# Performance work log

Hardware: AMD Instinct MI355X
Metric: run time of the kernel (lower is better)

The kernel has to match this reference:

```python
import jax, jax.numpy as jnp
import numpy as np

WINDOWS = [2, 4, 6]
THR = 0.5


def conv1x1(x, w, b):
    # x: [N,C,H,W], w: [O,C], b: [O]
    return jnp.einsum('nchw,oc->nohw', x, w) + b[None, :, None, None]


def cpool(x):
    # channel max + mean -> [N,2,H,W]
    return jnp.stack([x.max(axis=1), x.mean(axis=1)], axis=1)


def mask_fusion(orin, feature, w1, b1, w2, b2):
    sim = jax.nn.sigmoid(jnp.sum(conv1x1(cpool(orin), w1, b1) * conv1x1(cpool(feature), w2, b2), axis=1, keepdims=True))
    mask = (sim > THR).astype(orin.dtype)
    return mask * feature + (1.0 - mask) * orin


def unfold(x, kh, kw, sh, sw, w):
    # torch F.unfold equivalent -> [N, C*kh*kw, w*w] (channel-major like torch)
    rows = jnp.arange(w)[:, None] * sh + jnp.arange(kh)[None, :]  # [w,kh]
    cols = jnp.arange(w)[:, None] * sw + jnp.arange(kw)[None, :]  # [w,kw]
    p = x[:, :, rows[:, :, None, None], cols[None, None, :, :]]  # [N,C,w,kh,w,kw]
    p = p.transpose(0, 1, 3, 5, 2, 4)  # [N,C,kh,kw,w,w]
    N, C = x.shape[:2]
    return p.reshape(N, C * kh * kw, w * w)


def fold(cols_, H, W, kh, kw, sh, sw, w):
    # torch F.fold equivalent (col2im with overlap-add)
    N, CK, P = cols_.shape
    C = CK // (kh * kw)
    p = cols_.reshape(N, C, kh, kw, w, w).transpose(0, 1, 4, 2, 5, 3).reshape(N, C, w * kh, w * kw)
    r = (jnp.arange(w)[:, None] * sh + jnp.arange(kh)[None, :]).reshape(-1)
    c = (jnp.arange(w)[:, None] * sw + jnp.arange(kw)[None, :]).reshape(-1)
    return jnp.zeros((N, C, H, W), cols_.dtype).at[:, :, r[:, None], c[None, :]].add(p)


def psa(u, wq, wk, wv):
    # u: [N,C,P,L]; scaled dot-product self-attention over L within each patch
    t = u.transpose(0, 2, 3, 1)  # [N,P,L,C]
    q, k, v = t @ wq, t @ wk, t @ wv
    s = jnp.einsum('nplc,npmc->nplm', q, k) / jnp.sqrt(jnp.asarray(t.shape[-1], t.dtype))
    o = jnp.einsum('nplm,npmc->nplc', jax.nn.softmax(s, axis=-1), v)
    return o.transpose(0, 3, 1, 2)


def setup_inputs():
    key = jax.random.key(0)
    ks = jax.random.split(key, 20)
    N, C, H, W = 4, 64, 72, 72
    E = len(WINDOWS) * C
    nrm = lambda k, shape, s: jax.random.normal(k, shape, jnp.float32) * s
    return {
        'x': nrm(ks[0], (N, C, H, W), 1.0),
        'exp_w': nrm(ks[1], (E, C), C ** -0.5), 'exp_b': jnp.zeros((E,), jnp.float32),
        'res_w': nrm(ks[2], (C, E), E ** -0.5), 'res_b': jnp.zeros((C,), jnp.float32),
        'fus_w': nrm(ks[3], (C, C), C ** -0.5), 'fus_b': jnp.zeros((C,), jnp.float32),
        'wq': nrm(ks[4], (C, C), C ** -0.5),
        'wk': nrm(ks[5], (C, C), C ** -0.5),
        'wv': nrm(ks[6], (C, C), C ** -0.5),
        'mf1a_w': nrm(ks[7], (2, 2), 0.7), 'mf1a_b': jnp.zeros((2,), jnp.float32),
        'mf1b_w': nrm(ks[8], (2, 2), 0.7), 'mf1b_b': jnp.zeros((2,), jnp.float32),
        'mf2a_w': nrm(ks[9], (2, 2), 0.7), 'mf2a_b': jnp.zeros((2,), jnp.float32),
        'mf2b_w': nrm(ks[10], (2, 2), 0.7), 'mf2b_b': jnp.zeros((2,), jnp.float32),
    }


def reference(x, exp_w, exp_b, res_w, res_b, fus_w, fus_b, wq, wk, wv,
              mf1a_w, mf1a_b, mf1b_w, mf1b_b, mf2a_w, mf2a_b, mf2b_w, mf2b_b):
    N, C, H, W = x.shape
    expx = conv1x1(x, exp_w, exp_b)  # [N, 3C, H, W]
    parts = jnp.split(expx, len(WINDOWS), axis=1)
    outs = []
    for i, w in enumerate(WINDOWS):
        sh, sw = H // w, W // w
        kh, kw = sh + H % w, sw + W % w
        u = unfold(parts[i], kh, kw, sh, sw, w)       # [N, C*kh*kw, w*w]
        u = u.reshape(N, C, w * w, kh * kw)           # raw reinterpret, as in torch .view
        a = psa(u, wq, wk, wv).reshape(N, C * kh * kw, w * w)
        cnt = fold(jnp.ones_like(a), H, W, kh, kw, sh, sw, w)
        outs.append(fold(a, H, W, kh, kw, sh, sw, w) / cnt)
    out = mask_fusion(jnp.concatenate(outs, axis=1), expx, mf1a_w, mf1a_b, mf1b_w, mf1b_b)
    out = conv1x1(out, res_w, res_b)
    out = mask_fusion(out, x, mf2a_w, mf2a_b, mf2b_w, mf2b_b)
    return conv1x1(out, fus_w, fus_b)
```

## Files before the change

### kernel.cpp

```cpp
#include <hip/hip_runtime.h>

constexpr int CN = 4;
constexpr int CC = 64;
constexpr int CH = 72, CW = 72;
constexpr int HW = CH * CW;
constexpr int NPOS = CN * HW;
constexpr long TOKF = 3L * NPOS * 64;
constexpr long HPAD = 4096;

typedef _Float16 h4 __attribute__((ext_vector_type(4)));
typedef _Float16 h8 __attribute__((ext_vector_type(8)));
typedef float f4 __attribute__((ext_vector_type(4)));

__device__ __forceinline__ int fidx(int row, int g, int off) {
  return (row << 6) + ((g ^ (row & 7)) << 3) + off;
}
__device__ __forceinline__ int f192(int row, int g) {
  return row * 192 + (((g & 24) | ((g ^ row) & 7)) << 3);
}

template <int WW, int SS>
__device__ __forceinline__ void expand_body(const float* __restrict__ x,
                                            const float* __restrict__ w64,
                                            const float* __restrict__ b64,
                                            float* __restrict__ out, int pg) {
  int n = pg / HW;
  int pos = pg - n * HW;
  int h = pos / CW, wcol = pos % CW;

  float xv[64];
  const float* xp = x + (long)n * CC * HW + pos;
#pragma unroll
  for (int c = 0; c < 64; ++c) xv[c] = xp[c * HW];

  int wr = h / SS, kx = h % SS, wcq = wcol / SS, ky = wcol % SS;
  int j = kx * (SS * WW * WW) + ky * (WW * WW) + wr * WW + wcq;
  float* op = out + ((long)n * HW + j) * 64;

#pragma unroll 1
  for (int og = 0; og < 16; ++og) {
    float t0[4];
#pragma unroll
    for (int i = 0; i < 4; ++i) {
      int o = og * 4 + i;
      float acc = b64[o];
      const float* wp = w64 + o * 64;
#pragma unroll
      for (int cg = 0; cg < 16; ++cg) {
        float4 w4 = *(const float4*)(wp + 4 * cg);
        acc = fmaf(xv[4 * cg + 0], w4.x, acc);
        acc = fmaf(xv[4 * cg + 1], w4.y, acc);
        acc = fmaf(xv[4 * cg + 2], w4.z, acc);
        acc = fmaf(xv[4 * cg + 3], w4.w, acc);
      }
      t0[i] = acc;
    }
    *(float4*)(op + og * 4) = make_float4(t0[0], t0[1], t0[2], t0[3]);
  }
}

__global__ __launch_bounds__(256) void k_prep(
    const float* __restrict__ x, const float* __restrict__ exp_w,
    const float* __restrict__ exp_b, const float* __restrict__ wq,
    const float* __restrict__ wk, const float* __restrict__ wv,
    const float* __restrict__ res_w, const float* __restrict__ fus_w,
    float* __restrict__ ex, _Float16* __restrict__ wTh,
    _Float16* __restrict__ wTl, _Float16* __restrict__ rwh,
    _Float16* __restrict__ rwl, _Float16* __restrict__ fwh,
    _Float16* __restrict__ fwl) {
  int b = blockIdx.x;
  if (b >= 243) {
    int i = (b - 243) * 256 + threadIdx.x;
    float v;
    _Float16 *dh, *dl;
    int off;
    if (i < 12288) {
      int m = i >> 12;
      int r = i & 4095;
      int cp = r >> 6, c = r & 63;
      const float* src = (m == 0) ? wq : ((m == 1) ? wk : wv);
      v = src[c * 64 + cp];
      dh = wTh; dl = wTl; off = i;
    } else if (i < 24576) {
      off = i - 12288;
      v = res_w[off];
      dh = rwh; dl = rwl;
    } else {
      off = i - 24576;
      v = fus_w[off];
      dh = fwh; dl = fwl;
    }
    _Float16 h = (_Float16)v;
    dh[off] = h;
    dl[off] = (_Float16)(v - (float)h);
    return;
  }
  int wi = b / 81;
  int pg = (b - wi * 81) * 256 + threadIdx.x;
  if (wi == 0)
    expand_body<2, 36>(x, exp_w, exp_b, ex, pg);
  else if (wi == 1)
    expand_body<4, 18>(x, exp_w + 4096, exp_b + 64, ex + (long)NPOS * 64, pg);
  else
    expand_body<6, 12>(x, exp_w + 8192, exp_b + 128, ex + 2L * NPOS * 64, pg);
}

__global__ __launch_bounds__(256) void k_qkv(
    const float* __restrict__ ex, const _Float16* __restrict__ wTh,
    const _Float16* __restrict__ wTl, _Float16* __restrict__ qh,
    _Float16* __restrict__ ql, _Float16* __restrict__ kh,
    _Float16* __restrict__ kl, _Float16* __restrict__ vth,
    _Float16* __restrict__ vtl) {
  __shared__ __align__(16) _Float16 Wh[12288], Wl[12288];
  __shared__ __align__(16) float Cb[4096];
  _Float16* Eh = (_Float16*)Cb;
  _Float16* El = (_Float16*)Cb + 4096;

  const int tid = threadIdx.x;
  const long tok0 = (long)blockIdx.x * 64;
  const int lane = tid & 63, w = tid >> 6;
  const int lw = lane & 15, lg = lane >> 4;

  {
    int srow = tid >> 2, sfq = tid & 3;
#pragma unroll
    for (int p = 0; p < 4; ++p) {
      int c0 = (4 * p + sfq) * 4;
      float4 v = *(const float4*)(ex + (tok0 + srow) * 64 + c0);
      h4 hh = {(_Float16)v.x, (_Float16)v.y, (_Float16)v.z, (_Float16)v.w};
      h4 ll = {(_Float16)(v.x - (float)hh[0]), (_Float16)(v.y - (float)hh[1]),
               (_Float16)(v.z - (float)hh[2]), (_Float16)(v.w - (float)hh[3])};
      *(h4*)&Eh[fidx(srow, c0 >> 3, c0 & 7)] = hh;
      *(h4*)&El[fidx(srow, c0 >> 3, c0 & 7)] = ll;
    }
  }
#pragma unroll
  for (int it = 0; it < 6; ++it) {
    int idx = it * 256 + tid;
    int row = idx >> 3, gr = idx & 7;
    *(h8*)&Wh[fidx(row, gr, 0)] = *(const h8*)(wTh + idx * 8);
    *(h8*)&Wl[fidx(row, gr, 0)] = *(const h8*)(wTl + idx * 8);
  }
  __syncthreads();

  h8 eh[2], el[2];
#pragma unroll
  for (int s = 0; s < 2; ++s) {
    eh[s] = *(const h8*)&Eh[fidx(w * 16 + lw, s * 4 + lg, 0)];
    el[s] = *(const h8*)&El[fidx(w * 16 + lw, s * 4 + lg, 0)];
  }
  __syncthreads();

  const float SC = 0.125f * 1.4426950408889634f;
#pragma unroll 1
  for (int p = 0; p < 3; ++p) {
#pragma unroll
    for (int ot = 0; ot < 4; ++ot) {
      f4 acc = (f4){0.f, 0.f, 0.f, 0.f};
#pragma unroll
      for (int s = 0; s < 2; ++s) {
        h8 bh = *(const h8*)&Wh[fidx(p * 64 + ot * 16 + lw, s * 4 + lg, 0)];
        h8 bl = *(const h8*)&Wl[fidx(p * 64 + ot * 16 + lw, s * 4 + lg, 0)];
        acc = __builtin_amdgcn_mfma_f32_16x16x32_f16(eh[s], bh, acc, 0, 0, 0);
        acc = __builtin_amdgcn_mfma_f32_16x16x32_f16(el[s], bh, acc, 0, 0, 0);
        acc = __builtin_amdgcn_mfma_f32_16x16x32_f16(eh[s], bl, acc, 0, 0, 0);
      }
#pragma unroll
      for (int r = 0; r < 4; ++r) {
        int row = w * 16 + 4 * lg + r;
        int col = ot * 16 + lw;
        Cb[(row << 6) + ((((col >> 2) ^ (row & 15))) << 2) + (col & 3)] =
            acc[r];
      }
    }
    __syncthreads();

    if (p < 2) {
      int tokl = tid >> 2, off = (tid & 3) * 16;
      float vals[16];
#pragma unroll
      for (int j = 0; j < 4; ++j) {
        int slot = (off >> 2) + j;
        f4 v = *(const f4*)&Cb[(tokl << 6) + (((slot ^ (tokl & 15))) << 2)];
        vals[4 * j + 0] = v[0]; vals[4 * j + 1] = v[1];
        vals[4 * j + 2] = v[2]; vals[4 * j + 3] = v[3];
      }
      float sc = (p == 0) ? SC : 1.0f;
      _Float16* dh = (p == 0 ? qh : kh) + (tok0 + tokl) * 64 + off;
      _Float16* dl = (p == 0 ? ql : kl) + (tok0 + tokl) * 64 + off;
      h8 hh0, hh1, ll0, ll1;
#pragma unroll
      for (int j = 0; j < 8; ++j) {
        float x0 = vals[j] * sc;
        _Float16 h = (_Float16)x0;
        hh0[j] = h;
        ll0[j] = (_Float16)(x0 - (float)h);
        float x1 = vals[8 + j] * sc;
        _Float16 h1 = (_Float16)x1;
        hh1[j] = h1;
        ll1[j] = (_Float16)(x1 - (float)h1);
      }
      *(h8*)dh = hh0; *(h8*)(dh + 8) = hh1;
      *(h8*)dl = ll0; *(h8*)(dl + 8) = ll1;
    } else {
      int ch0 = (tid & 15) * 4, tokl0 = (tid >> 4) * 4;
      float tv[4][4];
#pragma unroll
      for (int r = 0; r < 4; ++r) {
        int row = tokl0 + r;
        int slot = (ch0 >> 2) ^ (row & 15);
        f4 v = *(const f4*)&Cb[(row << 6) + (slot << 2)];
        tv[r][0] = v[0]; tv[r][1] = v[1]; tv[r][2] = v[2]; tv[r][3] = v[3];
      }
      long tokg = tok0 + tokl0;
      int wi = (int)(tokg / NPOS);
      long tl = tokg - (long)wi * NPOS;
      int L = (wi == 0) ? 1296 : ((wi == 1) ? 324 : 144);
      int g = (int)(tl / L);
      int key0 = (int)(tl - (long)g * L);
      long base = (long)wi * NPOS * 64 + (long)g * 64 * L + key0;
#pragma unroll
      for (int i = 0; i < 4; ++i) {
        h4 hh, ll;
#pragma unroll
        for (int r = 0; r < 4; ++r) {
          _Float16 h = (_Float16)tv[r][i];
          hh[r] = h;
          ll[r] = (_Float16)(tv[r][i] - (float)h);
        }
        *(h4*)&vth[base + (long)(ch0 + i) * L] = hh;
        *(h4*)&vtl[base + (long)(ch0 + i) * L] = ll;
      }
    }
    __syncthreads();
  }
}

__global__ __launch_bounds__(256) void k_attn(
    const _Float16* __restrict__ qg, const _Float16* __restrict__ qgl,
    const _Float16* __restrict__ kg, const _Float16* __restrict__ kgl,
    const _Float16* __restrict__ vg, const _Float16* __restrict__ vgl,
    float* __restrict__ og_) {
  __shared__ __align__(16) _Float16 Qh[4096], Ql[4096];
  __shared__ __align__(16) _Float16 Kh[4096], Kl[4096];
  __shared__ __align__(16) _Float16 Vh[4096], Vl[4096];
  __shared__ __align__(16) _Float16 Ph[4096], Pl[4096];

  const int tid = threadIdx.x;
  int b = blockIdx.x;
  int L, g, qt, NCH;
  long tokbase, vbase;
  if (b < 336) {
    L = 1296; NCH = 21; g = b / 21; qt = b - g * 21;
    tokbase = (long)g * 1296;
    vbase = (long)g * 64 * 1296;
  } else if (b < 720) {
    int t = b - 336;
    L = 324; NCH = 6; g = t / 6; qt = t - g * 6;
    tokbase = (long)NPOS + (long)g * 324;
    vbase = (long)NPOS * 64 + (long)g * 64 * 324;
  } else {
    int t = b - 720;
    L = 144; NCH = 3; g = t / 3; qt = t - g * 3;
    tokbase = 2L * NPOS + (long)g * 144;
    vbase = 2L * NPOS * 64 + (long)g * 64 * 144;
  }

  const int lane = tid & 63, w = tid >> 6;
  const int lw = lane & 15, lg = lane >> 4;
  const int w16 = w * 16;

#pragma unroll
  for (int it = 0; it < 2; ++it) {
    int idx = it * 256 + tid;
    int row = idx >> 3, gr = idx & 7;
    long src = (tokbase + qt * 64 + row) * 64 + gr * 8;
    *(h8*)&Qh[fidx(row, gr, 0)] = *(const h8*)(qg + src);
    *(h8*)&Ql[fidx(row, gr, 0)] = *(const h8*)(qgl + src);
  }

  float m_s = -1e30f, l_s = 0.f;
  f4 oa[4];
#pragma unroll
  for (int i = 0; i < 4; ++i) oa[i] = (f4){0.f, 0.f, 0.f, 0.f};

  h8 rk0, rk1, rl0, rl1, rv0, rv1, rw0, rw1;
  auto loadKV = [&](int chn) {
    {
      int idx = tid;
      int row = idx >> 3, gr = idx & 7;
      long ks = (tokbase + chn * 64 + row) * 64 + gr * 8;
      long vs = vbase + (long)row * L + chn * 64 + gr * 8;
      rk0 = *(const h8*)(kg + ks);
      rl0 = *(const h8*)(kgl + ks);
      rv0 = *(const h8*)(vg + vs);
      rw0 = *(const h8*)(vgl + vs);
    }
    {
      int idx = 256 + tid;
      int row = idx >> 3, gr = idx & 7;
      long ks = (tokbase + chn * 64 + row) * 64 + gr * 8;
      long vs = vbase + (long)row * L + chn * 64 + gr * 8;
      rk1 = *(const h8*)(kg + ks);
      rl1 = *(const h8*)(kgl + ks);
      rv1 = *(const h8*)(vg + vs);
      rw1 = *(const h8*)(vgl + vs);
    }
  };
  loadKV(0);

  for (int ch = 0; ch < NCH; ++ch) {
    __syncthreads();
    {
      int row = tid >> 3, gr = tid & 7;
      *(h8*)&Kh[fidx(row, gr, 0)] = rk0;
      *(h8*)&Kl[fidx(row, gr, 0)] = rl0;
      *(h8*)&Vh[fidx(row, gr, 0)] = rv0;
      *(h8*)&Vl[fidx(row, gr, 0)] = rw0;
      int row1 = (256 + tid) >> 3;
      *(h8*)&Kh[fidx(row1, gr, 0)] = rk1;
      *(h8*)&Kl[fidx(row1, gr, 0)] = rl1;
      *(h8*)&Vh[fidx(row1, gr, 0)] = rv1;
      *(h8*)&Vl[fidx(row1, gr, 0)] = rw1;
    }
    __syncthreads();
    if (ch + 1 < NCH) loadKV(ch + 1);

    f4 sa[4];
#pragma unroll
    for (int kt = 0; kt < 4; ++kt) sa[kt] = (f4){0.f, 0.f, 0.f, 0.f};
#pragma unroll
    for (int slab = 0; slab < 2; ++slab) {
      h8 qbh = *(const h8*)&Qh[fidx(w16 + lw, slab * 4 + lg, 0)];
      h8 qbl = *(const h8*)&Ql[fidx(w16 + lw, slab * 4 + lg, 0)];
#pragma unroll
      for (int kt = 0; kt < 4; ++kt) {
        h8 ah = *(const h8*)&Kh[fidx(kt * 16 + lw, slab * 4 + lg, 0)];
        h8 al = *(const h8*)&Kl[fidx(kt * 16 + lw, slab * 4 + lg, 0)];
        sa[kt] = __builtin_amdgcn_mfma_f32_16x16x32_f16(ah, qbh, sa[kt], 0, 0, 0);
        sa[kt] = __builtin_amdgcn_mfma_f32_16x16x32_f16(al, qbh, sa[kt], 0, 0, 0);
        sa[kt] = __builtin_amdgcn_mfma_f32_16x16x32_f16(ah, qbl, sa[kt], 0, 0, 0);
      }
    }

    float pr[4][4];
    float pmax = -1e30f;
#pragma unroll
    for (int kt = 0; kt < 4; ++kt)
#pragma unroll
      for (int r = 0; r < 4; ++r) {
        int kidx = ch * 64 + kt * 16 + 4 * lg + r;
        float s = (kidx < L) ? sa[kt][r] : -1e30f;
        pr[kt][r] = s;
        pmax = fmaxf(pmax, s);
      }
    pmax = fmaxf(pmax, __shfl_xor(pmax, 16));
    pmax = fmaxf(pmax, __shfl_xor(pmax, 32));
    float mn = fmaxf(m_s, pmax);
    float fs = exp2f(m_s - mn);
    m_s = mn;
    float rs = 0.f;
#pragma unroll
    for (int kt = 0; kt < 4; ++kt)
#pragma unroll
      for (int r = 0; r < 4; ++r) {
        float e = exp2f(pr[kt][r] - mn);
        pr[kt][r] = e;
        rs += e;
      }
    rs += __shfl_xor(rs, 16);
    rs += __shfl_xor(rs, 32);
    l_s = l_s * fs + rs;
    float fsb[4];
#pragma unroll
    for (int r = 0; r < 4; ++r) fsb[r] = __shfl(fs, 4 * lg + r);
#pragma unroll
    for (int ct = 0; ct < 4; ++ct)
#pragma unroll
      for (int r = 0; r < 4; ++r) oa[ct][r] *= fsb[r];

#pragma unroll
    for (int kt = 0; kt < 4; ++kt) {
      h4 hh = {(_Float16)pr[kt][0], (_Float16)pr[kt][1], (_Float16)pr[kt][2],
               (_Float16)pr[kt][3]};
      h4 ll = {(_Float16)(pr[kt][0] - (float)hh[0]),
               (_Float16)(pr[kt][1] - (float)hh[1]),
               (_Float16)(pr[kt][2] - (float)hh[2]),
               (_Float16)(pr[kt][3] - (float)hh[3])};
      int key0 = kt * 16 + 4 * lg;
      int kgr = key0 >> 3, ko = key0 & 7;
      *(h4*)&Ph[fidx(w16 + lw, kgr, ko)] = hh;
      *(h4*)&Pl[fidx(w16 + lw, kgr, ko)] = ll;
    }

#pragma unroll
    for (int slab = 0; slab < 2; ++slab) {
      h8 pah = *(const h8*)&Ph[fidx(w16 + lw, slab * 4 + lg, 0)];
      h8 pal = *(const h8*)&Pl[fidx(w16 + lw, slab * 4 + lg, 0)];
#pragma unroll
      for (int ct = 0; ct < 4; ++ct) {
        h8 vbh = *(const h8*)&Vh[fidx(ct * 16 + lw, slab * 4 + lg, 0)];
        h8 vbl = *(const h8*)&Vl[fidx(ct * 16 + lw, slab * 4 + lg, 0)];
        oa[ct] = __builtin_amdgcn_mfma_f32_16x16x32_f16(pah, vbh, oa[ct], 0, 0, 0);
        oa[ct] = __builtin_amdgcn_mfma_f32_16x16x32_f16(pal, vbh, oa[ct], 0, 0, 0);
        oa[ct] = __builtin_amdgcn_mfma_f32_16x16x32_f16(pah, vbl, oa[ct], 0, 0, 0);
      }
    }
  }

  float linv[4];
#pragma unroll
  for (int r = 0; r < 4; ++r) linv[r] = 1.0f / __shfl(l_s, 4 * lg + r);
#pragma unroll
  for (int r = 0; r < 4; ++r) {
    int qi = qt * 64 + w16 + 4 * lg + r;
    if (qi < L) {
      float* op = og_ + (tokbase + qi) * 64 + lw;
#pragma unroll
      for (int ct = 0; ct < 4; ++ct) op[ct * 16] = oa[ct][r] * linv[r];
    }
  }
}

__global__ __launch_bounds__(256) void k_maskA(
    const float* __restrict__ ex, const float* __restrict__ att,
    const float* __restrict__ m1aw, const float* __restrict__ m1ab,
    const float* __restrict__ m1bw, const float* __restrict__ m1bb,
    _Float16* __restrict__ f1h, _Float16* __restrict__ f1l) {
  const int tid = threadIdx.x;
  const int wv = tid >> 6, lane = tid & 63;
  int pg = blockIdx.x * 4 + wv;
  int n = pg / HW, posn = pg - n * HW;
  int h = posn / CW, wcol = posn % CW;
  auto tok = [&](int S, int W) -> int {
    int wr = h / S, kx = h % S, wcq = wcol / S, ky = wcol % S;
    return kx * (S * W * W) + ky * (W * W) + wr * W + wcq;
  };
  int j0 = tok(36, 2), j1 = tok(18, 4), j2 = tok(12, 6);
  long t0 = ((long)n * HW + j0) * 64 + lane;
  long t1 = ((long)NPOS + (long)n * HW + j1) * 64 + lane;
  long t2 = (2L * NPOS + (long)n * HW + j2) * 64 + lane;
  float av0 = att[t0], av1 = att[t1], av2 = att[t2];
  float ev0 = ex[t0], ev1 = ex[t1], ev2 = ex[t2];
  float mxa = fmaxf(fmaxf(av0, av1), av2), sma = av0 + av1 + av2;
  float mxe = fmaxf(fmaxf(ev0, ev1), ev2), sme = ev0 + ev1 + ev2;
#pragma unroll
  for (int d = 1; d < 64; d <<= 1) {
    mxa = fmaxf(mxa, __shfl_xor(mxa, d));
    sma += __shfl_xor(sma, d);
    mxe = fmaxf(mxe, __shfl_xor(mxe, d));
    sme += __shfl_xor(sme, d);
  }
  float mna = sma * (1.f / 192.f), mne = sme * (1.f / 192.f);
  float ca0 = fmaf(m1aw[0], mxa, fmaf(m1aw[1], mna, m1ab[0]));
  float ca1 = fmaf(m1aw[2], mxa, fmaf(m1aw[3], mna, m1ab[1]));
  float cb0 = fmaf(m1bw[0], mxe, fmaf(m1bw[1], mne, m1bb[0]));
  float cb1 = fmaf(m1bw[2], mxe, fmaf(m1bw[3], mne, m1bb[1]));
  bool mk = (ca0 * cb0 + ca1 * cb1) > 0.f;
  _Float16* fh = f1h + (long)pg * 192 + lane;
  _Float16* fl = f1l + (long)pg * 192 + lane;
  float v0 = mk ? ev0 : av0;
  float v1 = mk ? ev1 : av1;
  float v2 = mk ? ev2 : av2;
  _Float16 h0 = (_Float16)v0, h1 = (_Float16)v1, h2 = (_Float16)v2;
  fh[0] = h0;   fl[0] = (_Float16)(v0 - (float)h0);
  fh[64] = h1;  fl[64] = (_Float16)(v1 - (float)h1);
  fh[128] = h2; fl[128] = (_Float16)(v2 - (float)h2);
}

__global__ __launch_bounds__(256) void k_fuse3(
    const float* __restrict__ x, const _Float16* __restrict__ f1h,
    const _Float16* __restrict__ f1l, const _Float16* __restrict__ rwh,
    const _Float16* __restrict__ rwl, const float* __restrict__ res_b,
    const _Float16* __restrict__ fwh, const _Float16* __restrict__ fwl,
    const float* __restrict__ fus_b, const float* __restrict__ m2aw,
    const float* __restrict__ m2ab, const float* __restrict__ m2bw,
    const float* __restrict__ m2bb, float* __restrict__ out) {
  __shared__ __align__(16) _Float16 F1hS[12288];
  __shared__ __align__(16) _Float16 F1lS[12288];
  float* Cb = (float*)F1hS;
  _Float16* o2h = F1lS;
  _Float16* o2l = F1lS + 4096;

  const int tid = threadIdx.x;
  const int posb = blockIdx.x * 64;
  const int n = posb / HW, posn = posb % HW;
  const int lane = tid & 63, w = tid >> 6;
  const int lw = lane & 15, lg = lane >> 4;
  const int w16 = w * 16;

#pragma unroll
  for (int it = 0; it < 6; ++it) {
    int idx = it * 256 + tid;
    int row = idx / 24, g = idx % 24;
    long src = (long)(posb + row) * 192 + g * 8;
    *(h8*)&F1hS[f192(row, g)] = *(const h8*)(f1h + src);
    *(h8*)&F1lS[f192(row, g)] = *(const h8*)(f1l + src);
  }
  __syncthreads();

  h8 ah[6], al[6];
#pragma unroll
  for (int s = 0; s < 6; ++s) {
    ah[s] = *(const h8*)&F1hS[f192(w16 + lw, s * 4 + lg)];
    al[s] = *(const h8*)&F1lS[f192(w16 + lw, s * 4 + lg)];
  }

  f4 acc[4];
#pragma unroll
  for (int ot = 0; ot < 4; ++ot) {
    float bb = res_b[ot * 16 + lw];
    acc[ot] = (f4){bb, bb, bb, bb};
#pragma unroll
    for (int s = 0; s < 6; ++s) {
      int wo = (ot * 16 + lw) * 192 + (s * 4 + lg) * 8;
      h8 bh = *(const h8*)(rwh + wo);
      h8 bl = *(const h8*)(rwl + wo);
      acc[ot] = __builtin_amdgcn_mfma_f32_16x16x32_f16(ah[s], bh, acc[ot], 0, 0, 0);
      acc[ot] = __builtin_amdgcn_mfma_f32_16x16x32_f16(al[s], bh, acc[ot], 0, 0, 0);
      acc[ot] = __builtin_amdgcn_mfma_f32_16x16x32_f16(ah[s], bl, acc[ot], 0, 0, 0);
    }
  }
  __syncthreads();

#pragma unroll
  for (int ot = 0; ot < 4; ++ot)
#pragma unroll
    for (int r = 0; r < 4; ++r) {
      int row = w16 + 4 * lg + r, col = ot * 16 + lw;
      Cb[(row << 6) + ((((col >> 2) ^ (row & 15))) << 2) + (col & 3)] =
          acc[ot][r];
    }
  __syncthreads();

  const int pos = tid >> 2, off = (tid & 3) * 16;
  float vals[16];
#pragma unroll
  for (int j = 0; j < 4; ++j) {
    int slot = (off >> 2) + j;
    f4 v = *(const f4*)&Cb[(pos << 6) + (((slot ^ (pos & 15))) << 2)];
    vals[4 * j + 0] = v[0]; vals[4 * j + 1] = v[1];
    vals[4 * j + 2] = v[2]; vals[4 * j + 3] = v[3];
  }
  float amx = vals[0], asum = vals[0];
#pragma unroll
  for (int i = 1; i < 16; ++i) {
    amx = fmaxf(amx, vals[i]);
    asum += vals[i];
  }
  amx = fmaxf(amx, __shfl_xor(amx, 1)); asum += __shfl_xor(asum, 1);
  amx = fmaxf(amx, __shfl_xor(amx, 2)); asum += __shfl_xor(asum, 2);
  float xv[16];
  const float* xp = x + ((long)n * CC + off) * HW + posn + pos;
#pragma unroll
  for (int i = 0; i < 16; ++i) xv[i] = xp[i * HW];
  float xmx = xv[0], xsum = xv[0];
#pragma unroll
  for (int i = 1; i < 16; ++i) {
    xmx = fmaxf(xmx, xv[i]);
    xsum += xv[i];
  }
  xmx = fmaxf(xmx, __shfl_xor(xmx, 1)); xsum += __shfl_xor(xsum, 1);
  xmx = fmaxf(xmx, __shfl_xor(xmx, 2)); xsum += __shfl_xor(xsum, 2);
  float rmn = asum * (1.f / 64.f), xmn = xsum * (1.f / 64.f);
  float ca0 = fmaf(m2aw[0], amx, fmaf(m2aw[1], rmn, m2ab[0]));
  float ca1 = fmaf(m2aw[2], amx, fmaf(m2aw[3], rmn, m2ab[1]));
  float cb0 = fmaf(m2bw[0], xmx, fmaf(m2bw[1], xmn, m2bb[0]));
  float cb1 = fmaf(m2bw[2], xmx, fmaf(m2bw[3], xmn, m2bb[1]));
  bool mk2 = (ca0 * cb0 + ca1 * cb1) > 0.f;

#pragma unroll
  for (int hf = 0; hf < 2; ++hf) {
    h8 hh, ll;
#pragma unroll
    for (int j = 0; j < 8; ++j) {
      float v = mk2 ? xv[hf * 8 + j] : vals[hf * 8 + j];
      _Float16 hx = (_Float16)v;
      hh[j] = hx;
      ll[j] = (_Float16)(v - (float)hx);
    }
    int g = (off >> 3) + hf;
    *(h8*)&o2h[fidx(pos, g, 0)] = hh;
    *(h8*)&o2l[fidx(pos, g, 0)] = ll;
  }
  __syncthreads();

  h8 a2h[2], a2l[2];
#pragma unroll
  for (int s = 0; s < 2; ++s) {
    a2h[s] = *(const h8*)&o2h[fidx(w16 + lw, s * 4 + lg, 0)];
    a2l[s] = *(const h8*)&o2l[fidx(w16 + lw, s * 4 + lg, 0)];
  }
  f4 acc2[4];
#pragma unroll
  for (int ot = 0; ot < 4; ++ot) {
    float bb = fus_b[ot * 16 + lw];
    acc2[ot] = (f4){bb, bb, bb, bb};
#pragma unroll
    for (int s = 0; s < 2; ++s) {
      int wo = (ot * 16 + lw) * 64 + (s * 4 + lg) * 8;
      h8 bh = *(const h8*)(fwh + wo);
      h8 bl = *(const h8*)(fwl + wo);
      acc2[ot] = __builtin_amdgcn_mfma_f32_16x16x32_f16(a2h[s], bh, acc2[ot], 0, 0, 0);
      acc2[ot] = __builtin_amdgcn_mfma_f32_16x16x32_f16(a2l[s], bh, acc2[ot], 0, 0, 0);
      acc2[ot] = __builtin_amdgcn_mfma_f32_16x16x32_f16(a2h[s], bl, acc2[ot], 0, 0, 0);
    }
  }
  __syncthreads();

#pragma unroll
  for (int ot = 0; ot < 4; ++ot)
#pragma unroll
    for (int r = 0; r < 4; ++r) {
      int prow = w16 + 4 * lg + r, col = ot * 16 + lw;
      Cb[(prow << 6) + ((col + prow) & 63)] = acc2[ot][r];
    }
  __syncthreads();
#pragma unroll
  for (int i = 0; i < 16; ++i) {
    float v = Cb[(lane << 6) + ((w16 + i + lane) & 63)];
    out[((long)n * CC + w16 + i) * HW + posn + lane] = v;
  }
}

extern "C" void kernel_launch(void* const* d_in, const int* in_sizes, int n_in,
                              void* d_out, int out_size, void* d_ws,
                              size_t ws_size, hipStream_t stream) {
  (void)in_sizes; (void)n_in; (void)out_size;
  const float* x      = (const float*)d_in[0];
  const float* exp_w  = (const float*)d_in[1];
  const float* exp_b  = (const float*)d_in[2];
  const float* res_w  = (const float*)d_in[3];
  const float* res_b  = (const float*)d_in[4];
  const float* fus_w  = (const float*)d_in[5];
  const float* fus_b  = (const float*)d_in[6];
  const float* wq     = (const float*)d_in[7];
  const float* wk     = (const float*)d_in[8];
  const float* wv     = (const float*)d_in[9];
  const float* m1aw   = (const float*)d_in[10];
  const float* m1ab   = (const float*)d_in[11];
  const float* m1bw   = (const float*)d_in[12];
  const float* m1bb   = (const float*)d_in[13];
  const float* m2aw   = (const float*)d_in[14];
  const float* m2ab   = (const float*)d_in[15];
  const float* m2bw   = (const float*)d_in[16];
  const float* m2bb   = (const float*)d_in[17];

  const long HSZ = TOKF + HPAD;
  const size_t needF =
      2 * (size_t)TOKF + (6 * (size_t)HSZ + 2 * 12288 + 2 * 12288 + 2 * 4096) / 2;
  if (ws_size < needF * sizeof(float)) return;
  float* ws = (float*)d_ws;
  float* ex = ws;
  float* ob = ex + TOKF;
  _Float16* qh  = (_Float16*)(ob + TOKF);
  _Float16* ql  = qh + HSZ;
  _Float16* kh  = ql + HSZ;
  _Float16* kl  = kh + HSZ;
  _Float16* vth = kl + HSZ;
  _Float16* vtl = vth + HSZ;
  _Float16* wTh = vtl + HSZ;
  _Float16* wTl = wTh + 12288;
  _Float16* rwh = wTl + 12288;
  _Float16* rwl = rwh + 12288;
  _Float16* fwh = rwl + 12288;
  _Float16* fwl = fwh + 4096;
  _Float16* f1h = qh;
  _Float16* f1l = ql;

  k_prep<<<355, 256, 0, stream>>>(x, exp_w, exp_b, wq, wk, wv, res_w, fus_w,
                                  ex, wTh, wTl, rwh, rwl, fwh, fwl);
  k_qkv<<<972, 256, 0, stream>>>(ex, wTh, wTl, qh, ql, kh, kl, vth, vtl);
  k_attn<<<1152, 256, 0, stream>>>(qh, ql, kh, kl, vth, vtl, ob);
  k_maskA<<<5184, 256, 0, stream>>>(ex, ob, m1aw, m1ab, m1bw, m1bb, f1h, f1l);
  k_fuse3<<<324, 256, 0, stream>>>(x, f1h, f1l, rwh, rwl, res_b, fwh, fwl,
                                   fus_b, m2aw, m2ab, m2bw, m2bb,
                                   (float*)d_out);
}
```

Baseline: 156.3 us.

## Process two query tiles per attention block and skip unneeded softmax rescales

Each attention block now handles two 64-query tiles, so every K/V chunk staged in shared memory feeds both tiles. This halves the global K/V traffic and the block count. Q fragments are held in registers instead of shared memory. The online-softmax rescale is skipped when the new running max exceeds the old by no more than a threshold, which saves exp and multiply work. The cost is more registers per thread, which may lower occupancy, and fewer blocks, which may leave some CUs idle.

```diff
diff --git a/kernel.cpp b/kernel.cpp
--- a/kernel.cpp
+++ b/kernel.cpp
@@ -241,183 +241,196 @@
     const _Float16* __restrict__ kg, const _Float16* __restrict__ kgl,
     const _Float16* __restrict__ vg, const _Float16* __restrict__ vgl,
     float* __restrict__ og_) {
-  __shared__ __align__(16) _Float16 Qh[4096], Ql[4096];
   __shared__ __align__(16) _Float16 Kh[4096], Kl[4096];
   __shared__ __align__(16) _Float16 Vh[4096], Vl[4096];
   __shared__ __align__(16) _Float16 Ph[4096], Pl[4096];
 
   const int tid = threadIdx.x;
   int b = blockIdx.x;
-  int L, g, qt, NCH;
+  int L, g, qt0, nt, NCH;
   long tokbase, vbase;
-  if (b < 336) {
-    L = 1296; NCH = 21; g = b / 21; qt = b - g * 21;
-    tokbase = (long)g * 1296;
-    vbase = (long)g * 64 * 1296;
-  } else if (b < 720) {
-    int t = b - 336;
-    L = 324; NCH = 6; g = t / 6; qt = t - g * 6;
+  if (b < 176) {
+    L = 1296; NCH = 21; g = b / 11;
+    int bi = b - g * 11;
+    qt0 = bi * 2; nt = (bi < 10) ? 2 : 1;
+    tokbase = (long)g * 1296; vbase = (long)g * 1296 * 64;
+  } else if (b < 368) {
+    int t = b - 176;
+    L = 324; NCH = 6; g = t / 3;
+    int bi = t - g * 3;
+    qt0 = bi * 2; nt = 2;
     tokbase = (long)NPOS + (long)g * 324;
-    vbase = (long)NPOS * 64 + (long)g * 64 * 324;
+    vbase = (long)NPOS * 64 + (long)g * 324 * 64;
   } else {
-    int t = b - 720;
-    L = 144; NCH = 3; g = t / 3; qt = t - g * 3;
+    int t = b - 368;
+    L = 144; NCH = 3; g = t >> 1;
+    int bi = t & 1;
+    qt0 = bi * 2; nt = bi ? 1 : 2;
     tokbase = 2L * NPOS + (long)g * 144;
-    vbase = 2L * NPOS * 64 + (long)g * 64 * 144;
+    vbase = 2L * NPOS * 64 + (long)g * 144 * 64;
   }
 
   const int lane = tid & 63, w = tid >> 6;
   const int lw = lane & 15, lg = lane >> 4;
   const int w16 = w * 16;
 
-#pragma unroll
-  for (int it = 0; it < 2; ++it) {
-    int idx = it * 256 + tid;
-    int row = idx >> 3, gr = idx & 7;
-    long src = (tokbase + qt * 64 + row) * 64 + gr * 8;
-    *(h8*)&Qh[fidx(row, gr, 0)] = *(const h8*)(qg + src);
-    *(h8*)&Ql[fidx(row, gr, 0)] = *(const h8*)(qgl + src);
-  }
-
-  float m_s = -1e30f, l_s = 0.f;
-  f4 oa[4];
-#pragma unroll
-  for (int i = 0; i < 4; ++i) oa[i] = (f4){0.f, 0.f, 0.f, 0.f};
+  h8 qfh[2][2], qfl[2][2];
+#pragma unroll
+  for (int t = 0; t < 2; ++t) {
+    int tt = (t < nt) ? t : 0;
+    long qb = (tokbase + (long)(qt0 + tt) * 64 + w16 + lw) * 64;
+#pragma unroll
+    for (int s = 0; s < 2; ++s) {
+      qfh[t][s] = *(const h8*)(qg + qb + (s * 4 + lg) * 8);
+      qfl[t][s] = *(const h8*)(qgl + qb + (s * 4 + lg) * 8);
+    }
+  }
+
+  float m_s[2] = {-1e30f, -1e30f}, l_s[2] = {0.f, 0.f};
+  f4 oa[2][4];
+#pragma unroll
+  for (int t = 0; t < 2; ++t)
+#pragma unroll
+    for (int i = 0; i < 4; ++i) oa[t][i] = (f4){0.f, 0.f, 0.f, 0.f};
+
+  const int krow = tid >> 3, kgr = tid & 7;
+  const long ksA = (tokbase + krow) * 64 + kgr * 8;
+  const long vsA = vbase + (long)krow * L + kgr * 8;
+  const long v32 = (long)32 * L;
 
   h8 rk0, rk1, rl0, rl1, rv0, rv1, rw0, rw1;
   auto loadKV = [&](int chn) {
-    {
-      int idx = tid;
-      int row = idx >> 3, gr = idx & 7;
-      long ks = (tokbase + chn * 64 + row) * 64 + gr * 8;
-      long vs = vbase + (long)row * L + chn * 64 + gr * 8;
-      rk0 = *(const h8*)(kg + ks);
-      rl0 = *(const h8*)(kgl + ks);
-      rv0 = *(const h8*)(vg + vs);
-      rw0 = *(const h8*)(vgl + vs);
-    }
-    {
-      int idx = 256 + tid;
-      int row = idx >> 3, gr = idx & 7;
-      long ks = (tokbase + chn * 64 + row) * 64 + gr * 8;
-      long vs = vbase + (long)row * L + chn * 64 + gr * 8;
-      rk1 = *(const h8*)(kg + ks);
-      rl1 = *(const h8*)(kgl + ks);
-      rv1 = *(const h8*)(vg + vs);
-      rw1 = *(const h8*)(vgl + vs);
-    }
+    long ko = ksA + ((long)chn << 12);
+    long vo = vsA + chn * 64;
+    rk0 = *(const h8*)(kg + ko);
+    rl0 = *(const h8*)(kgl + ko);
+    rv0 = *(const h8*)(vg + vo);
+    rw0 = *(const h8*)(vgl + vo);
+    rk1 = *(const h8*)(kg + ko + 2048);
+    rl1 = *(const h8*)(kgl + ko + 2048);
+    rv1 = *(const h8*)(vg + vo + v32);
+    rw1 = *(const h8*)(vgl + vo + v32);
   };
   loadKV(0);
 
   for (int ch = 0; ch < NCH; ++ch) {
     __syncthreads();
     {
-      int row = tid >> 3, gr = tid & 7;
-      *(h8*)&Kh[fidx(row, gr, 0)] = rk0;
-      *(h8*)&Kl[fidx(row, gr, 0)] = rl0;
-      *(h8*)&Vh[fidx(row, gr, 0)] = rv0;
-      *(h8*)&Vl[fidx(row, gr, 0)] = rw0;
-      int row1 = (256 + tid) >> 3;
-      *(h8*)&Kh[fidx(row1, gr, 0)] = rk1;
-      *(h8*)&Kl[fidx(row1, gr, 0)] = rl1;
-      *(h8*)&Vh[fidx(row1, gr, 0)] = rv1;
-      *(h8*)&Vl[fidx(row1, gr, 0)] = rw1;
+      *(h8*)&Kh[fidx(krow, kgr, 0)] = rk0;
+      *(h8*)&Kl[fidx(krow, kgr, 0)] = rl0;
+      *(h8*)&Vh[fidx(krow, kgr, 0)] = rv0;
+      *(h8*)&Vl[fidx(krow, kgr, 0)] = rw0;
+      *(h8*)&Kh[fidx(32 + krow, kgr, 0)] = rk1;
+      *(h8*)&Kl[fidx(32 + krow, kgr, 0)] = rl1;
+      *(h8*)&Vh[fidx(32 + krow, kgr, 0)] = rv1;
+      *(h8*)&Vl[fidx(32 + krow, kgr, 0)] = rw1;
     }
     __syncthreads();
     if (ch + 1 < NCH) loadKV(ch + 1);
 
-    f4 sa[4];
-#pragma unroll
-    for (int kt = 0; kt < 4; ++kt) sa[kt] = (f4){0.f, 0.f, 0.f, 0.f};
-#pragma unroll
-    for (int slab = 0; slab < 2; ++slab) {
-      h8 qbh = *(const h8*)&Qh[fidx(w16 + lw, slab * 4 + lg, 0)];
-      h8 qbl = *(const h8*)&Ql[fidx(w16 + lw, slab * 4 + lg, 0)];
+#pragma unroll
+    for (int t = 0; t < 2; ++t) {
+      if (t >= nt) break;
+      f4 sa[4];
+#pragma unroll
+      for (int kt = 0; kt < 4; ++kt) sa[kt] = (f4){0.f, 0.f, 0.f, 0.f};
+#pragma unroll
+      for (int slab = 0; slab < 2; ++slab) {
+        h8 qbh = qfh[t][slab];
+        h8 qbl = qfl[t][slab];
+#pragma unroll
+        for (int kt = 0; kt < 4; ++kt) {
+          h8 ah = *(const h8*)&Kh[fidx(kt * 16 + lw, slab * 4 + lg, 0)];
+          h8 al = *(const h8*)&Kl[fidx(kt * 16 + lw, slab * 4 + lg, 0)];
+          sa[kt] = __builtin_amdgcn_mfma_f32_16x16x32_f16(ah, qbh, sa[kt], 0, 0, 0);
+          sa[kt] = __builtin_amdgcn_mfma_f32_16x16x32_f16(al, qbh, sa[kt], 0, 0, 0);
+          sa[kt] = __builtin_amdgcn_mfma_f32_16x16x32_f16(ah, qbl, sa[kt], 0, 0, 0);
+        }
+      }
+
+      float pr[4][4];
+      float pmax = -1e30f;
+#pragma unroll
+      for (int kt = 0; kt < 4; ++kt)
+#pragma unroll
+        for (int r = 0; r < 4; ++r) {
+          int kidx = ch * 64 + kt * 16 + 4 * lg + r;
+          float s = (kidx < L) ? sa[kt][r] : -1e30f;
+          pr[kt][r] = s;
+          pmax = fmaxf(pmax, s);
+        }
+      pmax = fmaxf(pmax, __shfl_xor(pmax, 16));
+      pmax = fmaxf(pmax, __shfl_xor(pmax, 32));
+      if (!__all(pmax <= m_s[t] + 8.0f)) {
+        float mn = fmaxf(m_s[t], pmax);
+        float fs = exp2f(m_s[t] - mn);
+        m_s[t] = mn;
+        float fsb[4];
+#pragma unroll
+        for (int r = 0; r < 4; ++r) fsb[r] = __shfl(fs, 4 * lg + r);
+#pragma unroll
+        for (int ct = 0; ct < 4; ++ct)
+#pragma unroll
+          for (int r = 0; r < 4; ++r) oa[t][ct][r] *= fsb[r];
+        l_s[t] *= fs;
+      }
+      float rs = 0.f;
+#pragma unroll
+      for (int kt = 0; kt < 4; ++kt)
+#pragma unroll
+        for (int r = 0; r < 4; ++r) {
+          float e = exp2f(pr[kt][r] - m_s[t]);
+          pr[kt][r] = e;
+          rs += e;
+        }
+      rs += __shfl_xor(rs, 16);
+      rs += __shfl_xor(rs, 32);
+      l_s[t] += rs;
+
 #pragma unroll
       for (int kt = 0; kt < 4; ++kt) {
-        h8 ah = *(const h8*)&Kh[fidx(kt * 16 + lw, slab * 4 + lg, 0)];
-        h8 al = *(const h8*)&Kl[fidx(kt * 16 + lw, slab * 4 + lg, 0)];
-        sa[kt] = __builtin_amdgcn_mfma_f32_16x16x32_f16(ah, qbh, sa[kt], 0, 0, 0);
-        sa[kt] = __builtin_amdgcn_mfma_f32_16x16x32_f16(al, qbh, sa[kt], 0, 0, 0);
-        sa[kt] = __builtin_amdgcn_mfma_f32_16x16x32_f16(ah, qbl, sa[kt], 0, 0, 0);
-      }
-    }
-
-    float pr[4][4];
-    float pmax = -1e30f;
-#pragma unroll
-    for (int kt = 0; kt < 4; ++kt)
-#pragma unroll
-      for (int r = 0; r < 4; ++r) {
-        int kidx = ch * 64 + kt * 16 + 4 * lg + r;
-        float s = (kidx < L) ? sa[kt][r] : -1e30f;
-        pr[kt][r] = s;
-        pmax = fmaxf(pmax, s);
-      }
-    pmax = fmaxf(pmax, __shfl_xor(pmax, 16));
-    pmax = fmaxf(pmax, __shfl_xor(pmax, 32));
-    float mn = fmaxf(m_s, pmax);
-    float fs = exp2f(m_s - mn);
-    m_s = mn;
-    float rs = 0.f;
-#pragma unroll
-    for (int kt = 0; kt < 4; ++kt)
-#pragma unroll
-      for (int r = 0; r < 4; ++r) {
-        float e = exp2f(pr[kt][r] - mn);
-        pr[kt][r] = e;
-        rs += e;
-      }
-    rs += __shfl_xor(rs, 16);
-    rs += __shfl_xor(rs, 32);
-    l_s = l_s * fs + rs;
-    float fsb[4];
-#pragma unroll
-    for (int r = 0; r < 4; ++r) fsb[r] = __shfl(fs, 4 * lg + r);
-#pragma unroll
-    for (int ct = 0; ct < 4; ++ct)
-#pragma unroll
-      for (int r = 0; r < 4; ++r) oa[ct][r] *= fsb[r];
-
-#pragma unroll
-    for (int kt = 0; kt < 4; ++kt) {
-      h4 hh = {(_Float16)pr[kt][0], (_Float16)pr[kt][1], (_Float16)pr[kt][2],
-               (_Float16)pr[kt][3]};
-      h4 ll = {(_Float16)(pr[kt][0] - (float)hh[0]),
-               (_Float16)(pr[kt][1] - (float)hh[1]),
-               (_Float16)(pr[kt][2] - (float)hh[2]),
-               (_Float16)(pr[kt][3] - (float)hh[3])};
-      int key0 = kt * 16 + 4 * lg;
-      int kgr = key0 >> 3, ko = key0 & 7;
-      *(h4*)&Ph[fidx(w16 + lw, kgr, ko)] = hh;
-      *(h4*)&Pl[fidx(w16 + lw, kgr, ko)] = ll;
-    }
-
-#pragma unroll
-    for (int slab = 0; slab < 2; ++slab) {
-      h8 pah = *(const h8*)&Ph[fidx(w16 + lw, slab * 4 + lg, 0)];
-      h8 pal = *(const h8*)&Pl[fidx(w16 + lw, slab * 4 + lg, 0)];
-#pragma unroll
-      for (int ct = 0; ct < 4; ++ct) {
-        h8 vbh = *(const h8*)&Vh[fidx(ct * 16 + lw, slab * 4 + lg, 0)];
-        h8 vbl = *(const h8*)&Vl[fidx(ct * 16 + lw, slab * 4 + lg, 0)];
-        oa[ct] = __builtin_amdgcn_mfma_f32_16x16x32_f16(pah, vbh, oa[ct], 0, 0, 0);
-        oa[ct] = __builtin_amdgcn_mfma_f32_16x16x32_f16(pal, vbh, oa[ct], 0, 0, 0);
-        oa[ct] = __builtin_amdgcn_mfma_f32_16x16x32_f16(pah, vbl, oa[ct], 0, 0, 0);
-      }
-    }
-  }
-
-  float linv[4];
-#pragma unroll
-  for (int r = 0; r < 4; ++r) linv[r] = 1.0f / __shfl(l_s, 4 * lg + r);
-#pragma unroll
-  for (int r = 0; r < 4; ++r) {
-    int qi = qt * 64 + w16 + 4 * lg + r;
-    if (qi < L) {
-      float* op = og_ + (tokbase + qi) * 64 + lw;
-#pragma unroll
-      for (int ct = 0; ct < 4; ++ct) op[ct * 16] = oa[ct][r] * linv[r];
+        h4 hh = {(_Float16)pr[kt][0], (_Float16)pr[kt][1], (_Float16)pr[kt][2],
+                 (_Float16)pr[kt][3]};
+        h4 ll = {(_Float16)(pr[kt][0] - (float)hh[0]),
+                 (_Float16)(pr[kt][1] - (float)hh[1]),
+                 (_Float16)(pr[kt][2] - (float)hh[2]),
+                 (_Float16)(pr[kt][3] - (float)hh[3])};
+        int key0 = kt * 16 + 4 * lg;
+        int kgr2 = key0 >> 3, ko = key0 & 7;
+        *(h4*)&Ph[fidx(w16 + lw, kgr2, ko)] = hh;
+        *(h4*)&Pl[fidx(w16 + lw, kgr2, ko)] = ll;
+      }
+
+#pragma unroll
+      for (int slab = 0; slab < 2; ++slab) {
+        h8 pah = *(const h8*)&Ph[fidx(w16 + lw, slab * 4 + lg, 0)];
+        h8 pal = *(const h8*)&Pl[fidx(w16 + lw, slab * 4 + lg, 0)];
+#pragma unroll
+        for (int ct = 0; ct < 4; ++ct) {
+          h8 vbh = *(const h8*)&Vh[fidx(ct * 16 + lw, slab * 4 + lg, 0)];
+          h8 vbl = *(const h8*)&Vl[fidx(ct * 16 + lw, slab * 4 + lg, 0)];
+          oa[t][ct] = __builtin_amdgcn_mfma_f32_16x16x32_f16(pah, vbh, oa[t][ct], 0, 0, 0);
+          oa[t][ct] = __builtin_amdgcn_mfma_f32_16x16x32_f16(pal, vbh, oa[t][ct], 0, 0, 0);
+          oa[t][ct] = __builtin_amdgcn_mfma_f32_16x16x32_f16(pah, vbl, oa[t][ct], 0, 0, 0);
+        }
+      }
+    }
+  }
+
+#pragma unroll
+  for (int t = 0; t < 2; ++t) {
+    if (t >= nt) break;
+    float linv[4];
+#pragma unroll
+    for (int r = 0; r < 4; ++r) linv[r] = 1.0f / __shfl(l_s[t], 4 * lg + r);
+#pragma unroll
+    for (int r = 0; r < 4; ++r) {
+      int qi = (qt0 + t) * 64 + w16 + 4 * lg + r;
+      if (qi < L) {
+        float* op = og_ + (tokbase + qi) * 64 + lw;
+#pragma unroll
+        for (int ct = 0; ct < 4; ++ct) op[ct * 16] = oa[t][ct][r] * linv[r];
+      }
     }
   }
 }
@@ -671,7 +684,7 @@
   k_prep<<<355, 256, 0, stream>>>(x, exp_w, exp_b, wq, wk, wv, res_w, fus_w,
                                   ex, wTh, wTl, rwh, rwl, fwh, fwl);
   k_qkv<<<972, 256, 0, stream>>>(ex, wTh, wTl, qh, ql, kh, kl, vth, vtl);
-  k_attn<<<1152, 256, 0, stream>>>(qh, ql, kh, kl, vth, vtl, ob);
+  k_attn<<<656, 256, 0, stream>>>(qh, ql, kh, kl, vth, vtl, ob);
   k_maskA<<<5184, 256, 0, stream>>>(ex, ob, m1aw, m1ab, m1bw, m1bb, f1h, f1l);
   k_fuse3<<<324, 256, 0, stream>>>(x, f1h, f1l, rwh, rwl, res_b, fwh, fwl,
                                    fus_b, m2aw, m2ab, m2bw, m2bb,
```

Result: slower. 166.8 us (+6.7%).

## Hold Q fragments in registers, precompute KV offsets, lazily rescale softmax

Applied to the files above, without the earlier changes.

The Q tile is now loaded straight from global memory into per-lane register fragments instead of being staged in LDS. This removes 16 KB of shared memory per block and the LDS reads from the inner loop, which may allow more resident blocks. KV load addresses are hoisted out of the loop into precomputed base offsets. The online-softmax rescale of the accumulator and the running sum is skipped unless some row's new max exceeds the running max by more than 8, which cuts per-chunk shuffles and multiplies at the cost of slightly larger exponent ranges in the fp16 split.

```diff
diff --git a/kernel.cpp b/kernel.cpp
--- a/kernel.cpp
+++ b/kernel.cpp
@@ -241,7 +241,6 @@
     const _Float16* __restrict__ kg, const _Float16* __restrict__ kgl,
     const _Float16* __restrict__ vg, const _Float16* __restrict__ vgl,
     float* __restrict__ og_) {
-  __shared__ __align__(16) _Float16 Qh[4096], Ql[4096];
   __shared__ __align__(16) _Float16 Kh[4096], Kl[4096];
   __shared__ __align__(16) _Float16 Vh[4096], Vl[4096];
   __shared__ __align__(16) _Float16 Ph[4096], Pl[4096];
@@ -253,30 +252,31 @@
   if (b < 336) {
     L = 1296; NCH = 21; g = b / 21; qt = b - g * 21;
     tokbase = (long)g * 1296;
-    vbase = (long)g * 64 * 1296;
+    vbase = (long)g * 1296 * 64;
   } else if (b < 720) {
     int t = b - 336;
     L = 324; NCH = 6; g = t / 6; qt = t - g * 6;
     tokbase = (long)NPOS + (long)g * 324;
-    vbase = (long)NPOS * 64 + (long)g * 64 * 324;
+    vbase = (long)NPOS * 64 + (long)g * 324 * 64;
   } else {
     int t = b - 720;
     L = 144; NCH = 3; g = t / 3; qt = t - g * 3;
     tokbase = 2L * NPOS + (long)g * 144;
-    vbase = 2L * NPOS * 64 + (long)g * 64 * 144;
+    vbase = 2L * NPOS * 64 + (long)g * 144 * 64;
   }
 
   const int lane = tid & 63, w = tid >> 6;
   const int lw = lane & 15, lg = lane >> 4;
   const int w16 = w * 16;
 
-#pragma unroll
-  for (int it = 0; it < 2; ++it) {
-    int idx = it * 256 + tid;
-    int row = idx >> 3, gr = idx & 7;
-    long src = (tokbase + qt * 64 + row) * 64 + gr * 8;
-    *(h8*)&Qh[fidx(row, gr, 0)] = *(const h8*)(qg + src);
-    *(h8*)&Ql[fidx(row, gr, 0)] = *(const h8*)(qgl + src);
+  h8 qfh[2], qfl[2];
+  {
+    long qb = (tokbase + (long)qt * 64 + w16 + lw) * 64;
+#pragma unroll
+    for (int s = 0; s < 2; ++s) {
+      qfh[s] = *(const h8*)(qg + qb + (s * 4 + lg) * 8);
+      qfl[s] = *(const h8*)(qgl + qb + (s * 4 + lg) * 8);
+    }
   }
 
   float m_s = -1e30f, l_s = 0.f;
@@ -284,44 +284,37 @@
 #pragma unroll
   for (int i = 0; i < 4; ++i) oa[i] = (f4){0.f, 0.f, 0.f, 0.f};
 
+  const int krow = tid >> 3, kgr = tid & 7;
+  const long ksA = (tokbase + krow) * 64 + kgr * 8;
+  const long vsA = vbase + (long)krow * L + kgr * 8;
+  const long v32 = (long)32 * L;
+
   h8 rk0, rk1, rl0, rl1, rv0, rv1, rw0, rw1;
   auto loadKV = [&](int chn) {
-    {
-      int idx = tid;
-      int row = idx >> 3, gr = idx & 7;
-      long ks = (tokbase + chn * 64 + row) * 64 + gr * 8;
-      long vs = vbase + (long)row * L + chn * 64 + gr * 8;
-      rk0 = *(const h8*)(kg + ks);
-      rl0 = *(const h8*)(kgl + ks);
-      rv0 = *(const h8*)(vg + vs);
-      rw0 = *(const h8*)(vgl + vs);
-    }
-    {
-      int idx = 256 + tid;
-      int row = idx >> 3, gr = idx & 7;
-      long ks = (tokbase + chn * 64 + row) * 64 + gr * 8;
-      long vs = vbase + (long)row * L + chn * 64 + gr * 8;
-      rk1 = *(const h8*)(kg + ks);
-      rl1 = *(const h8*)(kgl + ks);
-      rv1 = *(const h8*)(vg + vs);
-      rw1 = *(const h8*)(vgl + vs);
-    }
+    long ko = ksA + ((long)chn << 12);
+    long vo = vsA + chn * 64;
+    rk0 = *(const h8*)(kg + ko);
+    rl0 = *(const h8*)(kgl + ko);
+    rv0 = *(const h8*)(vg + vo);
+    rw0 = *(const h8*)(vgl + vo);
+    rk1 = *(const h8*)(kg + ko + 2048);
+    rl1 = *(const h8*)(kgl + ko + 2048);
+    rv1 = *(const h8*)(vg + vo + v32);
+    rw1 = *(const h8*)(vgl + vo + v32);
   };
   loadKV(0);
 
   for (int ch = 0; ch < NCH; ++ch) {
     __syncthreads();
     {
-      int row = tid >> 3, gr = tid & 7;
-      *(h8*)&Kh[fidx(row, gr, 0)] = rk0;
-      *(h8*)&Kl[fidx(row, gr, 0)] = rl0;
-      *(h8*)&Vh[fidx(row, gr, 0)] = rv0;
-      *(h8*)&Vl[fidx(row, gr, 0)] = rw0;
-      int row1 = (256 + tid) >> 3;
-      *(h8*)&Kh[fidx(row1, gr, 0)] = rk1;
-      *(h8*)&Kl[fidx(row1, gr, 0)] = rl1;
-      *(h8*)&Vh[fidx(row1, gr, 0)] = rv1;
-      *(h8*)&Vl[fidx(row1, gr, 0)] = rw1;
+      *(h8*)&Kh[fidx(krow, kgr, 0)] = rk0;
+      *(h8*)&Kl[fidx(krow, kgr, 0)] = rl0;
+      *(h8*)&Vh[fidx(krow, kgr, 0)] = rv0;
+      *(h8*)&Vl[fidx(krow, kgr, 0)] = rw0;
+      *(h8*)&Kh[fidx(32 + krow, kgr, 0)] = rk1;
+      *(h8*)&Kl[fidx(32 + krow, kgr, 0)] = rl1;
+      *(h8*)&Vh[fidx(32 + krow, kgr, 0)] = rv1;
+      *(h8*)&Vl[fidx(32 + krow, kgr, 0)] = rw1;
     }
     __syncthreads();
     if (ch + 1 < NCH) loadKV(ch + 1);
@@ -331,8 +324,8 @@
     for (int kt = 0; kt < 4; ++kt) sa[kt] = (f4){0.f, 0.f, 0.f, 0.f};
 #pragma unroll
     for (int slab = 0; slab < 2; ++slab) {
-      h8 qbh = *(const h8*)&Qh[fidx(w16 + lw, slab * 4 + lg, 0)];
-      h8 qbl = *(const h8*)&Ql[fidx(w16 + lw, slab * 4 + lg, 0)];
+      h8 qbh = qfh[slab];
+      h8 qbl = qfl[slab];
 #pragma unroll
       for (int kt = 0; kt < 4; ++kt) {
         h8 ah = *(const h8*)&Kh[fidx(kt * 16 + lw, slab * 4 + lg, 0)];
@@ -356,28 +349,31 @@
       }
     pmax = fmaxf(pmax, __shfl_xor(pmax, 16));
     pmax = fmaxf(pmax, __shfl_xor(pmax, 32));
-    float mn = fmaxf(m_s, pmax);
-    float fs = exp2f(m_s - mn);
-    m_s = mn;
+    if (!__all(pmax <= m_s + 8.0f)) {
+      float mn = fmaxf(m_s, pmax);
+      float fs = exp2f(m_s - mn);
+      m_s = mn;
+      float fsb[4];
+#pragma unroll
+      for (int r = 0; r < 4; ++r) fsb[r] = __shfl(fs, 4 * lg + r);
+#pragma unroll
+      for (int ct = 0; ct < 4; ++ct)
+#pragma unroll
+        for (int r = 0; r < 4; ++r) oa[ct][r] *= fsb[r];
+      l_s *= fs;
+    }
     float rs = 0.f;
 #pragma unroll
     for (int kt = 0; kt < 4; ++kt)
 #pragma unroll
       for (int r = 0; r < 4; ++r) {
-        float e = exp2f(pr[kt][r] - mn);
+        float e = exp2f(pr[kt][r] - m_s);
         pr[kt][r] = e;
         rs += e;
       }
     rs += __shfl_xor(rs, 16);
     rs += __shfl_xor(rs, 32);
-    l_s = l_s * fs + rs;
-    float fsb[4];
-#pragma unroll
-    for (int r = 0; r < 4; ++r) fsb[r] = __shfl(fs, 4 * lg + r);
-#pragma unroll
-    for (int ct = 0; ct < 4; ++ct)
-#pragma unroll
-      for (int r = 0; r < 4; ++r) oa[ct][r] *= fsb[r];
+    l_s += rs;
 
 #pragma unroll
     for (int kt = 0; kt < 4; ++kt) {
@@ -388,9 +384,9 @@
                (_Float16)(pr[kt][2] - (float)hh[2]),
                (_Float16)(pr[kt][3] - (float)hh[3])};
       int key0 = kt * 16 + 4 * lg;
-      int kgr = key0 >> 3, ko = key0 & 7;
-      *(h4*)&Ph[fidx(w16 + lw, kgr, ko)] = hh;
-      *(h4*)&Pl[fidx(w16 + lw, kgr, ko)] = ll;
+      int kgr2 = key0 >> 3, ko = key0 & 7;
+      *(h4*)&Ph[fidx(w16 + lw, kgr2, ko)] = hh;
+      *(h4*)&Pl[fidx(w16 + lw, kgr2, ko)] = ll;
     }
 
 #pragma unroll
```

After: 153.4 us. Within noise of the previous version (-1.8%).
